# Performance work log

Measured on AMD Instinct MI355X. Metric: run time of the kernel, lower is better.

The kernel has to match this reference:

```python
import jax, jax.numpy as jnp
import numpy as np

K = 20            # num_control_points
OUT_H, OUT_W = 64, 256
MX, MY = 0.05, 0.05  # margins
EPS = 1e-6

def _ctrl_pts():
    half = K // 2
    x = np.linspace(MX, 1.0 - MX, half)
    top = np.stack([x, np.full(half, MY)], axis=1)
    bot = np.stack([x, np.full(half, 1.0 - MY)], axis=1)
    return np.concatenate([top, bot], axis=0)  # [K,2]

def _inv_delta(C):
    hat = np.linalg.norm(C[:, None] - C[None, :], axis=2)
    np.fill_diagonal(hat, 1.0)
    hat = hat ** 2 * np.log(hat)
    delta = np.concatenate([
        np.concatenate([np.ones((K, 1)), C, hat], axis=1),
        np.concatenate([np.zeros((2, 3)), C.T], axis=1),
        np.concatenate([np.zeros((1, 3)), np.ones((1, K))], axis=1)], axis=0)
    return np.linalg.inv(delta)  # [K+3, K+3]

def _g_lifted(C):
    gx = (np.arange(OUT_W) + 0.5) / OUT_W
    gy = (np.arange(OUT_H) + 0.5) / OUT_H
    G = np.stack(np.meshgrid(gx, gy), axis=2).reshape(-1, 2)  # [n,2]
    d = np.linalg.norm(G[:, None] - C[None, :], axis=2)       # [n,K]
    rbf = d ** 2 * np.log(d + EPS)
    return np.concatenate([np.ones((G.shape[0], 1)), G, rbf], axis=1)  # [n,K+3]

_C = _ctrl_pts()
INV_DELTA = jnp.asarray(_inv_delta(_C), jnp.float32)   # [K+3,K+3]
G_LIFTED = jnp.asarray(_g_lifted(_C), jnp.float32)     # [n,K+3], n=OUT_H*OUT_W


def setup_inputs() -> dict:
    key = jax.random.key(0)
    k1, k2 = jax.random.split(key)
    X = jax.random.uniform(k1, (128, 128, 512, 3), dtype=jnp.float32)
    ctrl = jax.random.uniform(k2, (128, K, 2), dtype=jnp.float32)
    return {"X": X, "input_control_points": ctrl}


def reference(X, input_control_points):
    B, H, W, ch = X.shape
    # --- TPS transform: T = inv_delta_C @ [Cp; 0_{3x2}] ---
    Cp0 = jnp.concatenate(
        [input_control_points, jnp.zeros((B, 3, 2), X.dtype)], axis=1)  # [B,K+3,2]
    T = jnp.einsum('ij,bjc->bic', INV_DELTA, Cp0)        # [B,K+3,2]
    Gp = jnp.einsum('ni,bic->bnc', G_LIFTED, T)          # [B,n,2] sampling grid

    # --- bilinear sampling ---
    Gx = jnp.clip(W * Gp[..., 0], 0.0, W - 2.0)
    Gy = jnp.clip(H * Gp[..., 1], 0.0, H - 2.0)
    x0 = jnp.floor(Gx).astype(jnp.int32); x1 = x0 + 1
    y0 = jnp.floor(Gy).astype(jnp.int32); y1 = y0 + 1
    b = jnp.arange(B)[:, None]                           # [B,1] broadcast over n
    I00 = X[b, y0, x0]                                   # [B,n,ch]
    I01 = X[b, y1, x0]
    I10 = X[b, y0, x1]
    I11 = X[b, y1, x1]
    fx0 = x0.astype(X.dtype); fx1 = x1.astype(X.dtype)
    fy0 = y0.astype(X.dtype); fy1 = y1.astype(X.dtype)
    w00 = (fx1 - Gx) * (fy1 - Gy)
    w01 = (fx1 - Gx) * (Gy - fy0)
    w10 = (Gx - fx0) * (fy1 - Gy)
    w11 = (Gx - fx0) * (Gy - fy0)
    pix = (w00[..., None] * I00 + w01[..., None] * I01
           + w10[..., None] * I10 + w11[..., None] * I11)  # [B,n,ch]
    return pix.reshape(B, OUT_H, OUT_W, ch)
```

## Files before the change

kernel.cpp:

```cpp
#include <hip/hip_runtime.h>
#include <math.h>

#define BATCH 128
#define IH    128
#define IW    512
#define CH    3
#define OH    64
#define OW    256
#define KCP   20
#define KP3   23

struct InvMat { float v[KP3 * KP3]; };

__global__ __launch_bounds__(64) void tps_T_kernel(InvMat inv,
                                                   const float* __restrict__ ctrl,
                                                   float* __restrict__ T) {
    int b = blockIdx.x;
    __shared__ float sc[KCP * 2];
    int t = threadIdx.x;
    if (t < KCP * 2) sc[t] = ctrl[b * KCP * 2 + t];
    __syncthreads();
    if (t < KP3 * 2) {
        int i = t >> 1, c = t & 1;
        double acc = 0.0;
        #pragma unroll
        for (int j = 0; j < KCP; ++j)
            acc += (double)inv.v[i * KP3 + j] * (double)sc[j * 2 + c];
        T[b * (KP3 * 2) + i * 2 + c] = (float)acc;
    }
}

__global__ __launch_bounds__(256) void tps_sample_kernel(const float* __restrict__ X,
                                                         const float* __restrict__ T,
                                                         float* __restrict__ out) {
    int bid = blockIdx.x;
    int b = bid >> 6;
    int y = bid & (OH - 1);
    int x = threadIdx.x;

    __shared__ float sT[KP3 * 2];
    if (x < KP3 * 2) sT[x] = T[b * (KP3 * 2) + x];
    __syncthreads();

    float gx = ((float)x + 0.5f) * (1.0f / OW);
    float gy = ((float)y + 0.5f) * (1.0f / OH);

    float px = sT[0] + gx * sT[2] + gy * sT[4];
    float py = sT[1] + gx * sT[3] + gy * sT[5];

    #pragma unroll
    for (int i = 0; i < KCP; ++i) {
        float cx = 0.05f + 0.1f * (float)(i % 10);
        float cy = (i < 10) ? 0.05f : 0.95f;
        float dx = gx - cx, dy = gy - cy;
        float d2 = dx * dx + dy * dy;
        float r = d2 * (0.5f * __logf(d2));
        px += r * sT[(3 + i) * 2 + 0];
        py += r * sT[(3 + i) * 2 + 1];
    }

    float Gx = fminf(fmaxf((float)IW * px, 0.0f), (float)(IW - 2));
    float Gy = fminf(fmaxf((float)IH * py, 0.0f), (float)(IH - 2));
    float fx0 = floorf(Gx), fy0 = floorf(Gy);
    int x0 = (int)fx0, y0 = (int)fy0;
    float fx = Gx - fx0, fy = Gy - fy0;

    float w00 = (1.0f - fx) * (1.0f - fy);
    float w10 = fx * (1.0f - fy);
    float w01 = (1.0f - fx) * fy;
    float w11 = fx * fy;

    const float* p00 = X + (((size_t)b * IH + y0) * IW + x0) * CH;
    const float* p01 = p00 + (size_t)IW * CH;

    float o0 = w00 * p00[0] + w10 * p00[3] + w01 * p01[0] + w11 * p01[3];
    float o1 = w00 * p00[1] + w10 * p00[4] + w01 * p01[1] + w11 * p01[4];
    float o2 = w00 * p00[2] + w10 * p00[5] + w01 * p01[2] + w11 * p01[5];

    float* o = out + ((size_t)bid * OW + x) * CH;
    o[0] = o0; o[1] = o1; o[2] = o2;
}

extern "C" void kernel_launch(void* const* d_in, const int* in_sizes, int n_in,
                              void* d_out, int out_size, void* d_ws, size_t ws_size,
                              hipStream_t stream) {
    const float* X    = (const float*)d_in[0];
    const float* ctrl = (const float*)d_in[1];
    float* out = (float*)d_out;
    float* T   = (float*)d_ws;

    double C[KCP][2];
    for (int j = 0; j < 10; ++j) {
        C[j][0]      = 0.05 + 0.1 * j;  C[j][1]      = 0.05;
        C[10 + j][0] = 0.05 + 0.1 * j;  C[10 + j][1] = 0.95;
    }

    double A[KP3][2 * KP3];
    for (int i = 0; i < KP3; ++i)
        for (int j = 0; j < 2 * KP3; ++j) A[i][j] = 0.0;

    for (int i = 0; i < KCP; ++i) {
        A[i][0] = 1.0; A[i][1] = C[i][0]; A[i][2] = C[i][1];
        for (int j = 0; j < KCP; ++j) {
            if (i == j) { A[i][3 + j] = 0.0; continue; }
            double dx = C[i][0] - C[j][0], dy = C[i][1] - C[j][1];
            double r2 = dx * dx + dy * dy;
            A[i][3 + j] = 0.5 * r2 * log(r2);
        }
    }
    for (int j = 0; j < KCP; ++j) {
        A[KCP + 0][3 + j] = C[j][0];
        A[KCP + 1][3 + j] = C[j][1];
        A[KCP + 2][3 + j] = 1.0;
    }
    for (int i = 0; i < KP3; ++i) A[i][KP3 + i] = 1.0;

    for (int k = 0; k < KP3; ++k) {
        int p = k; double best = fabs(A[k][k]);
        for (int i = k + 1; i < KP3; ++i)
            if (fabs(A[i][k]) > best) { best = fabs(A[i][k]); p = i; }
        if (p != k)
            for (int j = 0; j < 2 * KP3; ++j) { double t = A[k][j]; A[k][j] = A[p][j]; A[p][j] = t; }
        double pv = A[k][k];
        for (int j = 0; j < 2 * KP3; ++j) A[k][j] /= pv;
        for (int i = 0; i < KP3; ++i) {
            if (i == k) continue;
            double m = A[i][k];
            if (m == 0.0) continue;
            for (int j = 0; j < 2 * KP3; ++j) A[i][j] -= m * A[k][j];
        }
    }

    InvMat inv;
    for (int i = 0; i < KP3; ++i)
        for (int j = 0; j < KP3; ++j)
            inv.v[i * KP3 + j] = (float)A[i][KP3 + j];

    tps_T_kernel<<<BATCH, 64, 0, stream>>>(inv, ctrl, T);
    tps_sample_kernel<<<BATCH * OH, 256, 0, stream>>>(X, T, out);
}
```

Before: 166.2 us.

## Fuse TPS transform into sampling kernel with XCD-aware batch mapping

Merges the per-batch T computation into the sampling kernel, so every block recomputes its batch's 23x2 transform in shared memory in float instead of double. This removes one kernel launch and the global round trip for T. Block IDs are remapped so that all blocks of one batch land on the same XCD, which is meant to improve L2 reuse of the input image. Output stores become nontemporal. The cost is redundant T computation in every block and a change from double to float accumulation, which can alter rounding.

```diff
diff --git a/kernel.cpp b/kernel.cpp
--- a/kernel.cpp
+++ b/kernel.cpp
@@ -12,34 +12,30 @@
 
 struct InvMat { float v[KP3 * KP3]; };
 
-__global__ __launch_bounds__(64) void tps_T_kernel(InvMat inv,
-                                                   const float* __restrict__ ctrl,
-                                                   float* __restrict__ T) {
-    int b = blockIdx.x;
+__global__ __launch_bounds__(256) void tps_fused_kernel(InvMat inv,
+                                                        const float* __restrict__ ctrl,
+                                                        const float* __restrict__ X,
+                                                        float* __restrict__ out) {
+    int bid = blockIdx.x;
+    int xcd  = bid & 7;
+    int slot = bid >> 3;
+    int y = slot & (OH - 1);
+    int b = ((slot >> 6) << 3) | xcd;
+
     __shared__ float sc[KCP * 2];
-    int t = threadIdx.x;
-    if (t < KCP * 2) sc[t] = ctrl[b * KCP * 2 + t];
+    __shared__ float sT[KP3 * 2];
+    int x = threadIdx.x;
+
+    if (x < KCP * 2) sc[x] = ctrl[b * KCP * 2 + x];
     __syncthreads();
-    if (t < KP3 * 2) {
-        int i = t >> 1, c = t & 1;
-        double acc = 0.0;
+    if (x < KP3 * 2) {
+        int i = x >> 1, c = x & 1;
+        float acc = 0.0f;
         #pragma unroll
         for (int j = 0; j < KCP; ++j)
-            acc += (double)inv.v[i * KP3 + j] * (double)sc[j * 2 + c];
-        T[b * (KP3 * 2) + i * 2 + c] = (float)acc;
+            acc += inv.v[i * KP3 + j] * sc[j * 2 + c];
+        sT[x] = acc;
     }
-}
-
-__global__ __launch_bounds__(256) void tps_sample_kernel(const float* __restrict__ X,
-                                                         const float* __restrict__ T,
-                                                         float* __restrict__ out) {
-    int bid = blockIdx.x;
-    int b = bid >> 6;
-    int y = bid & (OH - 1);
-    int x = threadIdx.x;
-
-    __shared__ float sT[KP3 * 2];
-    if (x < KP3 * 2) sT[x] = T[b * (KP3 * 2) + x];
     __syncthreads();
 
     float gx = ((float)x + 0.5f) * (1.0f / OW);
@@ -77,8 +73,10 @@
     float o1 = w00 * p00[1] + w10 * p00[4] + w01 * p01[1] + w11 * p01[4];
     float o2 = w00 * p00[2] + w10 * p00[5] + w01 * p01[2] + w11 * p01[5];
 
-    float* o = out + ((size_t)bid * OW + x) * CH;
-    o[0] = o0; o[1] = o1; o[2] = o2;
+    float* o = out + (((size_t)b * OH + y) * OW + x) * CH;
+    __builtin_nontemporal_store(o0, o + 0);
+    __builtin_nontemporal_store(o1, o + 1);
+    __builtin_nontemporal_store(o2, o + 2);
 }
 
 extern "C" void kernel_launch(void* const* d_in, const int* in_sizes, int n_in,
@@ -87,7 +85,6 @@
     const float* X    = (const float*)d_in[0];
     const float* ctrl = (const float*)d_in[1];
     float* out = (float*)d_out;
-    float* T   = (float*)d_ws;
 
     double C[KCP][2];
     for (int j = 0; j < 10; ++j) {
@@ -136,6 +133,5 @@
         for (int j = 0; j < KP3; ++j)
             inv.v[i * KP3 + j] = (float)A[i][KP3 + j];
 
-    tps_T_kernel<<<BATCH, 64, 0, stream>>>(inv, ctrl, T);
-    tps_sample_kernel<<<BATCH * OH, 256, 0, stream>>>(X, T, out);
+    tps_fused_kernel<<<BATCH * OH, 256, 0, stream>>>(inv, ctrl, X, out);
 }
```

Measured after the change: 162.8 us. 2.1% less time.
